# Optimization experiments

Hardware: AMD Instinct MI355X
Metric: run time of the kernel (lower is better)

## Reference

```python
import jax, jax.numpy as jnp
import numpy as np

B, N, M, C = 8, 2048, 2048, 512


def setup_inputs() -> dict:
    key = jax.random.key(0)
    ks = jax.random.split(key, 10)
    s = 1.0 / np.sqrt(C)
    dec_embed = jax.random.normal(ks[0], (B, N, C), dtype=jnp.float32)
    enc_embed = jax.random.normal(ks[1], (B, M, C), dtype=jnp.float32)
    trans_mat = (jax.random.uniform(ks[2], (B, N, M)) < 0.5).astype(jnp.float32)
    Wv = jax.random.uniform(ks[3], (C, C), minval=-s, maxval=s, dtype=jnp.float32)
    bv = jax.random.uniform(ks[4], (C,), minval=-s, maxval=s, dtype=jnp.float32)
    W1 = jax.random.uniform(ks[5], (C, C), minval=-s, maxval=s, dtype=jnp.float32)
    b1 = jax.random.uniform(ks[6], (C,), minval=-s, maxval=s, dtype=jnp.float32)
    W2 = jax.random.uniform(ks[7], (C, C), minval=-s, maxval=s, dtype=jnp.float32)
    b2 = jax.random.uniform(ks[8], (C,), minval=-s, maxval=s, dtype=jnp.float32)
    return {"dec_embed": dec_embed, "enc_embed": enc_embed, "trans_mat": trans_mat,
            "Wv": Wv, "bv": bv, "W1": W1, "b1": b1, "W2": W2, "b2": b2}


def reference(dec_embed, enc_embed, trans_mat, Wv, bv, W1, b1, W2, b2):
    # scores [B,N,M], elementwise-masked by trans_mat
    attn = jnp.einsum('bnc,bmc->bnm', dec_embed, enc_embed) * trans_mat
    # NONSTANDARD masked softmax: zeros participate in softmax (exp(0)=1 in denom),
    # then positions where attn==0 are re-zeroed.
    sm = jax.nn.softmax(attn, axis=-1)
    attn = jnp.where(attn != 0, sm, jnp.zeros((), attn.dtype))
    v = enc_embed @ Wv + bv                      # [B,M,C]
    v = jnp.tanh(jnp.einsum('bnm,bmc->bnc', attn, v))  # [B,N,C]
    g = dec_embed * v + dec_embed                # tanh-gate + residual
    h = jax.nn.relu(g @ W1 + b1)                 # Mlp fc1 + ReLU (drop=0)
    return h @ W2 + b2                           # Mlp fc2
```

## Files before the change

### kernel.cpp

```cpp
#include <hip/hip_runtime.h>
#include <math.h>

#define Bb 8
#define Nn 2048
#define Mm 2048
#define Cc 512

typedef __attribute__((ext_vector_type(8))) _Float16 hfrag;
typedef __attribute__((ext_vector_type(4))) float f4;
typedef __attribute__((ext_vector_type(4))) _Float16 h4;

__device__ __forceinline__ void gld16(const void* g, void* l) {
    __builtin_amdgcn_global_load_lds(
        (const __attribute__((address_space(1))) void*)g,
        (__attribute__((address_space(3))) void*)l, 16, 0, 0);
}

template<int EPI, int BN, int SWZ>
__global__ __launch_bounds__(256) void gemm_mfma(
    const _Float16* __restrict__ Ah, long sA, int lda,
    const _Float16* __restrict__ Bh, long sB, int ldb,
    const float* __restrict__ aux, long sAux, int ldaux,
    const _Float16* __restrict__ aux2,
    float* __restrict__ mlal,
    void* __restrict__ Cout, long sC, int ldc, int K, int GX)
{
    constexpr int NI = (BN == 128) ? 4 : 2;
    constexpr int NQ = (512 + BN * 4) / 256;

    __shared__ _Float16 As[128 * 32];
    __shared__ _Float16 Bs[BN * 32];

    int bx, by, bz;
    if (SWZ == 1) {
        const int id = blockIdx.x;
        bz = id & 7; bx = (id >> 3) % GX; by = (id >> 3) / GX;
    } else if (SWZ == 2) {
        const int id = blockIdx.x;
        bz = 0; bx = (id >> 3) % GX; by = (id & 7) + 8 * ((id >> 3) / GX);
    } else {
        bx = blockIdx.x; by = blockIdx.y; bz = blockIdx.z;
    }

    const _Float16* A0 = Ah + (size_t)bz * sA;
    const _Float16* B0 = Bh + (size_t)bz * sB;

    const int tid  = threadIdx.x;
    const int wv   = tid >> 6;
    const int ln   = tid & 63;
    const int wx   = (BN == 128) ? (wv & 1) : 0;
    const int wy   = (BN == 128) ? (wv >> 1) : wv;
    const int lcol = ln & 15, quad = ln >> 4;
    const int row0w = wy * (NI * 16);
    const int col0w = wx * 64;

    const int rowBase = by * 128;
    const int colBase = bx * BN;

    f4 acc[NI][4];
    const f4 z4 = {0.f, 0.f, 0.f, 0.f};
    #pragma unroll
    for (int i = 0; i < NI; ++i)
        #pragma unroll
        for (int j = 0; j < 4; ++j) acc[i][j] = z4;

    const float* alb = (EPI == 2) ? (mlal + (size_t)bz * (2048 * 32)) : nullptr;

    for (int k0 = 0; k0 < K; k0 += 32) {
        __syncthreads();
        #pragma unroll
        for (int q = 0; q < NQ; ++q) {
            const int c0 = q * 256 + wv * 64;
            const int c  = c0 + ln;
            if (c0 < 512) {
                const int r  = c >> 2;
                const int ko = (c & 3) * 8;
                gld16(A0 + (size_t)(rowBase + r) * lda + k0 + ko, &As[c0 * 8]);
            } else {
                const int cb = c - 512;
                const int r  = cb >> 2;
                const int ko = (cb & 3) * 8;
                gld16(B0 + (size_t)(colBase + r) * ldb + k0 + ko, &Bs[(c0 - 512) * 8]);
            }
        }
        __syncthreads();

        hfrag af[NI], bf_[4];
        const int aoff = quad * 8;
        #pragma unroll
        for (int i = 0; i < NI; ++i)
            af[i]  = *(const hfrag*)&As[(row0w + i * 16 + lcol) * 32 + aoff];
        #pragma unroll
        for (int j = 0; j < 4; ++j)
            bf_[j] = *(const hfrag*)&Bs[(col0w + j * 16 + lcol) * 32 + aoff];

        if (EPI == 2) {
            const int t = k0 >> 6;
            #pragma unroll
            for (int i = 0; i < NI; ++i) {
                const int ar = rowBase + row0w + i * 16 + lcol;
                const _Float16 s = (_Float16)alb[(size_t)ar * 32 + t];
                af[i] = af[i] * s;
            }
        }

        #pragma unroll
        for (int i = 0; i < NI; ++i)
            #pragma unroll
            for (int j = 0; j < 4; ++j)
                acc[i][j] = __builtin_amdgcn_mfma_f32_16x16x32_f16(af[i], bf_[j], acc[i][j], 0, 0, 0);
    }

    const int crow0 = rowBase + row0w + quad * 4;
    const int ccol0 = colBase + col0w + lcol;

    if (EPI == 0) {
        _Float16* E = (_Float16*)Cout + (size_t)bz * sC;
        const float* Mk = aux + (size_t)bz * sAux;
        #pragma unroll
        for (int i = 0; i < NI; ++i)
            #pragma unroll
            for (int j = 0; j < 4; ++j)
                #pragma unroll
                for (int r = 0; r < 4; ++r) {
                    const int row = crow0 + i * 16 + r;
                    const int col = ccol0 + j * 16;
                    acc[i][j][r] *= Mk[(size_t)row * ldaux + col];
                }
        const int t = bx * 2 + wx;
        #pragma unroll
        for (int i = 0; i < NI; ++i) {
            #pragma unroll
            for (int r = 0; r < 4; ++r) {
                float m0 = fmaxf(fmaxf(acc[i][0][r], acc[i][1][r]),
                                 fmaxf(acc[i][2][r], acc[i][3][r]));
                #pragma unroll
                for (int off = 1; off <= 8; off <<= 1)
                    m0 = fmaxf(m0, __shfl_xor(m0, off, 64));
                float l0 = 0.f;
                const int row = crow0 + i * 16 + r;
                #pragma unroll
                for (int j = 0; j < 4; ++j) {
                    const float s = acc[i][j][r];
                    const float e = __expf(s - m0);
                    l0 += e;
                    E[(size_t)row * ldc + (ccol0 + j * 16)] =
                        (s == 0.f) ? (_Float16)0.f : (_Float16)e;
                }
                #pragma unroll
                for (int off = 1; off <= 8; off <<= 1)
                    l0 += __shfl_xor(l0, off, 64);
                if ((ln & 15) == 0) {
                    float2 p; p.x = m0; p.y = l0;
                    ((float2*)mlal)[((size_t)bz * 2048 + row) * 32 + t] = p;
                }
            }
        }
    } else if (EPI == 1) {
        _Float16* C = (_Float16*)Cout;
        #pragma unroll
        for (int j = 0; j < 4; ++j) {
            const int col = ccol0 + j * 16;
            const float bi = aux[col];
            #pragma unroll
            for (int i = 0; i < NI; ++i) {
                const int rowb = crow0 + i * 16;
                const int bb = rowb >> 11, ml = rowb & 2047;
                h4 st;
                #pragma unroll
                for (int r = 0; r < 4; ++r) st[r] = (_Float16)(acc[i][j][r] + bi);
                *(h4*)(C + (size_t)bb * ((size_t)Cc * Mm) + (size_t)col * Mm + ml) = st;
            }
        }
    } else if (EPI == 2) {
        _Float16* C = (_Float16*)Cout + (size_t)bz * sC;
        const _Float16* Dg = aux2 + (size_t)bz * sC;
        #pragma unroll
        for (int i = 0; i < NI; ++i)
            #pragma unroll
            for (int j = 0; j < 4; ++j)
                #pragma unroll
                for (int r = 0; r < 4; ++r) {
                    const int row = crow0 + i * 16 + r;
                    const int col = ccol0 + j * 16;
                    const float a = acc[i][j][r];
                    const float th = 1.f - 2.f / (__expf(2.f * a) + 1.f);
                    const float g = (float)Dg[(size_t)row * ldaux + col] * (1.f + th);
                    C[(size_t)row * ldc + col] = (_Float16)g;
                }
    } else if (EPI == 3) {
        _Float16* C = (_Float16*)Cout;
        #pragma unroll
        for (int i = 0; i < NI; ++i)
            #pragma unroll
            for (int j = 0; j < 4; ++j) {
                const int col = ccol0 + j * 16;
                const float bi = aux[col];
                #pragma unroll
                for (int r = 0; r < 4; ++r) {
                    const int row = crow0 + i * 16 + r;
                    C[(size_t)row * ldc + col] = (_Float16)fmaxf(acc[i][j][r] + bi, 0.f);
                }
            }
    } else {
        float* C = (float*)Cout;
        #pragma unroll
        for (int i = 0; i < NI; ++i)
            #pragma unroll
            for (int j = 0; j < 4; ++j) {
                const int col = ccol0 + j * 16;
                const float bi = aux[col];
                #pragma unroll
                for (int r = 0; r < 4; ++r) {
                    const int row = crow0 + i * 16 + r;
                    C[(size_t)row * ldc + col] = acc[i][j][r] + bi;
                }
            }
    }
}

__global__ __launch_bounds__(64) void combine_kernel(
    const float* __restrict__ mlq, float* __restrict__ alpha)
{
    const int row = blockIdx.x * 64 + threadIdx.x;
    const float2* ml = (const float2*)mlq + (size_t)row * 32;
    float mt[32], lt[32];
    float m = -1e30f;
    #pragma unroll
    for (int t = 0; t < 32; ++t) {
        float2 p = ml[t];
        mt[t] = p.x; lt[t] = p.y;
        m = fmaxf(m, p.x);
    }
    float et[32], l = 0.f;
    #pragma unroll
    for (int t = 0; t < 32; ++t) {
        et[t] = __expf(mt[t] - m);
        l += lt[t] * et[t];
    }
    const float inv = 1.f / l;
    float* ap = alpha + (size_t)row * 32;
    #pragma unroll
    for (int t = 0; t < 32; ++t) ap[t] = et[t] * inv;
}

__global__ __launch_bounds__(256) void sconv(const float* __restrict__ x,
                                             _Float16* __restrict__ o)
{
    const size_t i = (size_t)blockIdx.x * 256 + threadIdx.x;
    f4 v = ((const f4*)x)[i];
    h4 hh;
    #pragma unroll
    for (int k = 0; k < 4; ++k) hh[k] = (_Float16)v[k];
    ((h4*)o)[i] = hh;
}

__global__ __launch_bounds__(256) void wconv(const float* s0, const float* s1, const float* s2,
                                             _Float16* d0, _Float16* d1, _Float16* d2)
{
    const float* Sm = blockIdx.z == 0 ? s0 : blockIdx.z == 1 ? s1 : s2;
    _Float16* D = blockIdx.z == 0 ? d0 : blockIdx.z == 1 ? d1 : d2;
    __shared__ float t[32][33];
    const int x = threadIdx.x & 31, y = threadIdx.x >> 5;
    const int gx = blockIdx.x * 32, gy = blockIdx.y * 32;
    #pragma unroll
    for (int yy = y; yy < 32; yy += 8)
        t[yy][x] = Sm[(size_t)(gy + yy) * 512 + gx + x];
    __syncthreads();
    #pragma unroll
    for (int yy = y; yy < 32; yy += 8)
        D[(size_t)(gx + yy) * 512 + gy + x] = (_Float16)t[x][yy];
}

extern "C" void kernel_launch(void* const* d_in, const int* in_sizes, int n_in,
                              void* d_out, int out_size, void* d_ws, size_t ws_size,
                              hipStream_t stream)
{
    const float* dec   = (const float*)d_in[0];
    const float* enc   = (const float*)d_in[1];
    const float* trans = (const float*)d_in[2];
    const float* Wv = (const float*)d_in[3];
    const float* bv = (const float*)d_in[4];
    const float* W1 = (const float*)d_in[5];
    const float* b1 = (const float*)d_in[6];
    const float* W2 = (const float*)d_in[7];
    const float* b2 = (const float*)d_in[8];

    char* ws = (char*)d_ws;
    _Float16* e     = (_Float16*)ws;
    float*    mlq   = (float*)(ws + 0x4000000);
    float*    alpha = (float*)(ws + 0x4400000);
    _Float16* dec_h = (_Float16*)(ws + 0x4600000);
    _Float16* Wvt   = (_Float16*)(ws + 0x5600000);
    _Float16* W1t   = Wvt + 262144;
    _Float16* W2t   = Wvt + 524288;
    _Float16* vT    = (_Float16*)(ws + 0x5800000);
    _Float16* g     = (_Float16*)(ws + 0x6800000);
    _Float16* h     = (_Float16*)(ws + 0x7800000);
    _Float16* enc_h = (_Float16*)d_out;

    sconv<<<dim3(8192), 256, 0, stream>>>(dec, dec_h);
    sconv<<<dim3(8192), 256, 0, stream>>>(enc, enc_h);
    wconv<<<dim3(16, 16, 3), 256, 0, stream>>>(Wv, W1, W2, Wvt, W1t, W2t);

    gemm_mfma<0, 128, 1><<<dim3(2048), 256, 0, stream>>>(
        dec_h, (long)Nn * Cc, 512,
        enc_h, (long)Mm * Cc, 512,
        trans, (long)Nn * Mm, 2048, nullptr, mlq,
        e, (long)Nn * Mm, 2048, 512, 16);

    combine_kernel<<<dim3(256), 64, 0, stream>>>(mlq, alpha);

    gemm_mfma<1, 64, 2><<<dim3(1024), 256, 0, stream>>>(
        enc_h, 0, 512, Wvt, 0, 512, bv, 0, 0, nullptr, nullptr,
        vT, 0, 0, 512, 8);

    gemm_mfma<2, 128, 1><<<dim3(512), 256, 0, stream>>>(
        e, (long)Nn * Mm, 2048,
        vT, (long)Cc * Mm, 2048,
        nullptr, 0, 512, dec_h, alpha,
        g, (long)Nn * Cc, 512, 2048, 4);

    gemm_mfma<3, 64, 2><<<dim3(1024), 256, 0, stream>>>(
        g, 0, 512, W1t, 0, 512, b1, 0, 0, nullptr, nullptr,
        h, 0, 512, 512, 8);

    gemm_mfma<4, 64, 2><<<dim3(1024), 256, 0, stream>>>(
        h, 0, 512, W2t, 0, 512, b2, 0, 0, nullptr, nullptr,
        d_out, 0, 512, 512, 8);
}
```

Before: 466.8 us.

## Swap GEMM operand roles so epilogues write contiguous h4/f4 vectors

Every GEMM now runs in transposed form (C^T = B^T A^T) by swapping the A and B operands. Each lane's four accumulator rows then map to contiguous memory, so the mask loads and the E, g, h and output stores become 4-wide vector accesses instead of scalar ones. The softmax partial max and sum reductions now run across quads rather than lanes, and the alpha rescale moves to the B fragments, loaded once per 64-wide K chunk. Grid shapes and swizzles change to match, which shifts L2 reuse patterns, and the partial-stat layout changes.

```diff
diff --git a/kernel.cpp b/kernel.cpp
--- a/kernel.cpp
+++ b/kernel.cpp
@@ -39,7 +39,7 @@
         const int id = blockIdx.x;
         bz = 0; bx = (id >> 3) % GX; by = (id & 7) + 8 * ((id >> 3) / GX);
     } else {
-        bx = blockIdx.x; by = blockIdx.y; bz = blockIdx.z;
+        bx = blockIdx.x; by = blockIdx.y; bz = 0;
     }
 
     const _Float16* A0 = Ah + (size_t)bz * sA;
@@ -65,6 +65,7 @@
         for (int j = 0; j < 4; ++j) acc[i][j] = z4;
 
     const float* alb = (EPI == 2) ? (mlal + (size_t)bz * (2048 * 32)) : nullptr;
+    _Float16 als[4] = {(_Float16)0.f, (_Float16)0.f, (_Float16)0.f, (_Float16)0.f};
 
     for (int k0 = 0; k0 < K; k0 += 32) {
         __syncthreads();
@@ -95,13 +96,16 @@
             bf_[j] = *(const hfrag*)&Bs[(col0w + j * 16 + lcol) * 32 + aoff];
 
         if (EPI == 2) {
-            const int t = k0 >> 6;
-            #pragma unroll
-            for (int i = 0; i < NI; ++i) {
-                const int ar = rowBase + row0w + i * 16 + lcol;
-                const _Float16 s = (_Float16)alb[(size_t)ar * 32 + t];
-                af[i] = af[i] * s;
-            }
+            if ((k0 & 63) == 0) {
+                const int t = k0 >> 6;
+                #pragma unroll
+                for (int j = 0; j < 4; ++j) {
+                    const int n = colBase + col0w + j * 16 + lcol;
+                    als[j] = (_Float16)alb[(size_t)n * 32 + t];
+                }
+            }
+            #pragma unroll
+            for (int j = 0; j < 4; ++j) bf_[j] = bf_[j] * als[j];
         }
 
         #pragma unroll
@@ -118,42 +122,45 @@
         _Float16* E = (_Float16*)Cout + (size_t)bz * sC;
         const float* Mk = aux + (size_t)bz * sAux;
         #pragma unroll
-        for (int i = 0; i < NI; ++i)
-            #pragma unroll
-            for (int j = 0; j < 4; ++j)
+        for (int i = 0; i < NI; ++i) {
+            const int m0r = crow0 + i * 16;
+            #pragma unroll
+            for (int j = 0; j < 4; ++j) {
+                const int n = ccol0 + j * 16;
+                const f4 mk = *(const f4*)(Mk + (size_t)n * ldaux + m0r);
+                #pragma unroll
+                for (int r = 0; r < 4; ++r) acc[i][j][r] *= mk[r];
+            }
+        }
+        const int t = (rowBase + row0w) >> 6;
+        #pragma unroll
+        for (int j = 0; j < 4; ++j) {
+            const int n = ccol0 + j * 16;
+            float mx = acc[0][j][0];
+            #pragma unroll
+            for (int i = 0; i < NI; ++i)
+                #pragma unroll
+                for (int r = 0; r < 4; ++r) mx = fmaxf(mx, acc[i][j][r]);
+            mx = fmaxf(mx, __shfl_xor(mx, 16, 64));
+            mx = fmaxf(mx, __shfl_xor(mx, 32, 64));
+            float l0 = 0.f;
+            #pragma unroll
+            for (int i = 0; i < NI; ++i) {
+                h4 ev;
                 #pragma unroll
                 for (int r = 0; r < 4; ++r) {
-                    const int row = crow0 + i * 16 + r;
-                    const int col = ccol0 + j * 16;
-                    acc[i][j][r] *= Mk[(size_t)row * ldaux + col];
+                    const float s = acc[i][j][r];
+                    const float e = __expf(s - mx);
+                    l0 += e;
+                    ev[r] = (s == 0.f) ? (_Float16)0.f : (_Float16)e;
                 }
-        const int t = bx * 2 + wx;
-        #pragma unroll
-        for (int i = 0; i < NI; ++i) {
-            #pragma unroll
-            for (int r = 0; r < 4; ++r) {
-                float m0 = fmaxf(fmaxf(acc[i][0][r], acc[i][1][r]),
-                                 fmaxf(acc[i][2][r], acc[i][3][r]));
-                #pragma unroll
-                for (int off = 1; off <= 8; off <<= 1)
-                    m0 = fmaxf(m0, __shfl_xor(m0, off, 64));
-                float l0 = 0.f;
-                const int row = crow0 + i * 16 + r;
-                #pragma unroll
-                for (int j = 0; j < 4; ++j) {
-                    const float s = acc[i][j][r];
-                    const float e = __expf(s - m0);
-                    l0 += e;
-                    E[(size_t)row * ldc + (ccol0 + j * 16)] =
-                        (s == 0.f) ? (_Float16)0.f : (_Float16)e;
-                }
-                #pragma unroll
-                for (int off = 1; off <= 8; off <<= 1)
-                    l0 += __shfl_xor(l0, off, 64);
-                if ((ln & 15) == 0) {
-                    float2 p; p.x = m0; p.y = l0;
-                    ((float2*)mlal)[((size_t)bz * 2048 + row) * 32 + t] = p;
-                }
+                *(h4*)(E + (size_t)n * ldc + crow0 + i * 16) = ev;
+            }
+            l0 += __shfl_xor(l0, 16, 64);
+            l0 += __shfl_xor(l0, 32, 64);
+            if (quad == 0) {
+                float2 p; p.x = mx; p.y = l0;
+                ((float2*)mlal)[((size_t)bz * 2048 + n) * 32 + t] = p;
             }
         }
     } else if (EPI == 1) {
@@ -176,46 +183,53 @@
         _Float16* C = (_Float16*)Cout + (size_t)bz * sC;
         const _Float16* Dg = aux2 + (size_t)bz * sC;
         #pragma unroll
-        for (int i = 0; i < NI; ++i)
-            #pragma unroll
-            for (int j = 0; j < 4; ++j)
+        for (int i = 0; i < NI; ++i) {
+            const int c0 = crow0 + i * 16;
+            #pragma unroll
+            for (int j = 0; j < 4; ++j) {
+                const int n = ccol0 + j * 16;
+                const h4 dv = *(const h4*)(Dg + (size_t)n * ldc + c0);
+                h4 gv;
                 #pragma unroll
                 for (int r = 0; r < 4; ++r) {
-                    const int row = crow0 + i * 16 + r;
-                    const int col = ccol0 + j * 16;
                     const float a = acc[i][j][r];
                     const float th = 1.f - 2.f / (__expf(2.f * a) + 1.f);
-                    const float g = (float)Dg[(size_t)row * ldaux + col] * (1.f + th);
-                    C[(size_t)row * ldc + col] = (_Float16)g;
+                    gv[r] = (_Float16)((float)dv[r] * (1.f + th));
                 }
+                *(h4*)(C + (size_t)n * ldc + c0) = gv;
+            }
+        }
     } else if (EPI == 3) {
         _Float16* C = (_Float16*)Cout;
         #pragma unroll
-        for (int i = 0; i < NI; ++i)
+        for (int i = 0; i < NI; ++i) {
+            const int c0 = crow0 + i * 16;
+            const f4 bi = *(const f4*)(aux + c0);
             #pragma unroll
             for (int j = 0; j < 4; ++j) {
-                const int col = ccol0 + j * 16;
-                const float bi = aux[col];
-                #pragma unroll
-                for (int r = 0; r < 4; ++r) {
-                    const int row = crow0 + i * 16 + r;
-                    C[(size_t)row * ldc + col] = (_Float16)fmaxf(acc[i][j][r] + bi, 0.f);
-                }
-            }
+                const int n = ccol0 + j * 16;
+                h4 hv;
+                #pragma unroll
+                for (int r = 0; r < 4; ++r)
+                    hv[r] = (_Float16)fmaxf(acc[i][j][r] + bi[r], 0.f);
+                *(h4*)(C + (size_t)n * ldc + c0) = hv;
+            }
+        }
     } else {
         float* C = (float*)Cout;
         #pragma unroll
-        for (int i = 0; i < NI; ++i)
+        for (int i = 0; i < NI; ++i) {
+            const int c0 = crow0 + i * 16;
+            const f4 bi = *(const f4*)(aux + c0);
             #pragma unroll
             for (int j = 0; j < 4; ++j) {
-                const int col = ccol0 + j * 16;
-                const float bi = aux[col];
-                #pragma unroll
-                for (int r = 0; r < 4; ++r) {
-                    const int row = crow0 + i * 16 + r;
-                    C[(size_t)row * ldc + col] = acc[i][j][r] + bi;
-                }
-            }
+                const int n = ccol0 + j * 16;
+                f4 ov;
+                #pragma unroll
+                for (int r = 0; r < 4; ++r) ov[r] = acc[i][j][r] + bi[r];
+                *(f4*)(C + (size_t)n * ldc + c0) = ov;
+            }
+        }
     }
 }
 
@@ -304,8 +318,8 @@
     wconv<<<dim3(16, 16, 3), 256, 0, stream>>>(Wv, W1, W2, Wvt, W1t, W2t);
 
     gemm_mfma<0, 128, 1><<<dim3(2048), 256, 0, stream>>>(
+        enc_h, (long)Mm * Cc, 512,
         dec_h, (long)Nn * Cc, 512,
-        enc_h, (long)Mm * Cc, 512,
         trans, (long)Nn * Mm, 2048, nullptr, mlq,
         e, (long)Nn * Mm, 2048, 512, 16);
 
@@ -316,16 +330,16 @@
         vT, 0, 0, 512, 8);
 
     gemm_mfma<2, 128, 1><<<dim3(512), 256, 0, stream>>>(
+        vT, (long)Cc * Mm, 2048,
         e, (long)Nn * Mm, 2048,
-        vT, (long)Cc * Mm, 2048,
         nullptr, 0, 512, dec_h, alpha,
-        g, (long)Nn * Cc, 512, 2048, 4);
-
-    gemm_mfma<3, 64, 2><<<dim3(1024), 256, 0, stream>>>(
-        g, 0, 512, W1t, 0, 512, b1, 0, 0, nullptr, nullptr,
-        h, 0, 512, 512, 8);
-
-    gemm_mfma<4, 64, 2><<<dim3(1024), 256, 0, stream>>>(
-        h, 0, 512, W2t, 0, 512, b2, 0, 0, nullptr, nullptr,
-        d_out, 0, 512, 512, 8);
-}
+        g, (long)Nn * Cc, 512, 2048, 16);
+
+    gemm_mfma<3, 64, 0><<<dim3(256, 4), 256, 0, stream>>>(
+        W1t, 0, 512, g, 0, 512, b1, 0, 0, nullptr, nullptr,
+        h, 0, 512, 512, 0);
+
+    gemm_mfma<4, 64, 0><<<dim3(256, 4), 256, 0, stream>>>(
+        W2t, 0, 512, h, 0, 512, b2, 0, 0, nullptr, nullptr,
+        d_out, 0, 512, 512, 0);
+}
```

New measurement: 460.1 us. No clear change (-1.4%).
